# Kernel tuning notes

Hardware: AMD Instinct MI355X
Metric: run time of the kernel (lower is better)

The kernel has to match this reference:

```python
import jax, jax.numpy as jnp
import numpy as np
import math

B, T, C = 2, 2048, 1024
N_HEAD = 16
HEAD_DIM = C // N_HEAD


def setup_inputs() -> dict:
    key = jax.random.key(0)
    k1, k2, k3 = jax.random.split(key, 3)
    x = jax.random.normal(k1, (B, T, C), dtype=jnp.float32)
    # causal mask: positions where mask == 0 get -inf
    mask = jnp.tril(jnp.ones((T, T), dtype=bool))[None, None, :, :]
    W_attn = jax.random.normal(k2, (C, 3 * C), dtype=jnp.float32) * (1.0 / math.sqrt(C))
    b_attn = jnp.zeros((3 * C,), dtype=jnp.float32)
    W_proj = jax.random.normal(k3, (C, C), dtype=jnp.float32) * (1.0 / math.sqrt(C))
    b_proj = jnp.zeros((C,), dtype=jnp.float32)
    return {"x": x, "mask": mask, "W_attn": W_attn, "b_attn": b_attn,
            "W_proj": W_proj, "b_proj": b_proj}


def reference(x, mask, W_attn, b_attn, W_proj, b_proj):
    Bx, Tx, Cx = x.shape
    qkv = x @ W_attn + b_attn                      # [B,T,3C]
    q, k, v = jnp.split(qkv, 3, axis=2)
    # [B,T,C] -> [B,H,T,D]
    q = q.reshape(Bx, Tx, N_HEAD, HEAD_DIM).transpose(0, 2, 1, 3)
    k = k.reshape(Bx, Tx, N_HEAD, HEAD_DIM).transpose(0, 2, 1, 3)
    v = v.reshape(Bx, Tx, N_HEAD, HEAD_DIM).transpose(0, 2, 1, 3)
    scale = 1.0 / math.sqrt(HEAD_DIM)
    att = jnp.einsum('bhqd,bhkd->bhqk', q, k) * scale   # [B,H,T,T]
    att = jnp.where(mask, att, -jnp.inf)
    att = jax.nn.softmax(att, axis=-1)
    y = jnp.einsum('bhqk,bhkd->bhqd', att, v)            # [B,H,T,D]
    y = y.transpose(0, 2, 1, 3).reshape(Bx, Tx, Cx)      # [B,T,C]
    return y @ W_proj + b_proj
```

## Files before the change

### kernel.cpp

```cpp
#include <hip/hip_runtime.h>
#include <hip/hip_bf16.h>
#include <cstdint>

typedef unsigned short u16;
typedef unsigned int u32;
typedef unsigned long long u64;
using f32x4 = __attribute__((ext_vector_type(4))) float;
using s16x8 = __attribute__((ext_vector_type(8))) short;
using u32x4 = __attribute__((ext_vector_type(4))) u32;

#define NB 2
#define NT 2048
#define NC 1024
#define NH 16
#define HD 64

__device__ __forceinline__ u16 f2b(float f) {
    unsigned u = __float_as_uint(f);
    unsigned r = (u + 0x7FFFu + ((u >> 16) & 1u)) >> 16;
    return (u16)r;
}

__device__ __forceinline__ u32 cvtpk(float a, float b) {
    u32 r;
    asm("v_cvt_pk_bf16_f32 %0, %1, %2" : "=v"(r) : "v"(a), "v"(b));
    return r;
}
__device__ __forceinline__ void swap32(u32& a, u32& b) {
    asm("v_permlane32_swap_b32 %0, %1" : "+v"(a), "+v"(b));
}
__device__ __forceinline__ void swap16(u32& a, u32& b) {
    asm("v_permlane16_swap_b32 %0, %1" : "+v"(a), "+v"(b));
}

__device__ __forceinline__ void gl_lds16(const void* g, const void* l) {
    __builtin_amdgcn_global_load_lds(
        (const __attribute__((address_space(1))) unsigned int*)g,
        (__attribute__((address_space(3))) unsigned int*)l, 16, 0, 0);
}

__global__ __launch_bounds__(256) void conv_bf16(const float* __restrict__ in,
                                                 u16* __restrict__ out, int n4) {
    int i = blockIdx.x * 256 + threadIdx.x;
    if (i >= n4) return;
    float4 v = ((const float4*)in)[i];
    u64 pack = (u64)f2b(v.x) | ((u64)f2b(v.y) << 16) |
               ((u64)f2b(v.z) << 32) | ((u64)f2b(v.w) << 48);
    ((u64*)out)[i] = pack;
}

__global__ __launch_bounds__(256) void transpose_bf16(const float* __restrict__ W,
                                                      u16* __restrict__ Wt,
                                                      int K, int N) {
    __shared__ u16 s[64][65];
    const int n0 = blockIdx.x * 64, k0 = blockIdx.y * 64;
    const int t = threadIdx.x;
    const int tr = t >> 4, tc4 = (t & 15) * 4;
#pragma unroll
    for (int i = 0; i < 4; i++) {
        int r = tr + i * 16;
        float4 v = *(const float4*)&W[(size_t)(k0 + r) * N + n0 + tc4];
        s[r][tc4 + 0] = f2b(v.x);
        s[r][tc4 + 1] = f2b(v.y);
        s[r][tc4 + 2] = f2b(v.z);
        s[r][tc4 + 3] = f2b(v.w);
    }
    __syncthreads();
#pragma unroll
    for (int i = 0; i < 4; i++) {
        int nl = tr + i * 16;
        u64 pack = (u64)s[tc4 + 0][nl] | ((u64)s[tc4 + 1][nl] << 16) |
                   ((u64)s[tc4 + 2][nl] << 32) | ((u64)s[tc4 + 3][nl] << 48);
        *(u64*)&Wt[(size_t)(n0 + nl) * K + k0 + tc4] = pack;
    }
}

template <int OUT_BF16>
__global__ __launch_bounds__(256) void gemm_bt(const u16* __restrict__ A,
                                               const u16* __restrict__ Bt,
                                               const float* __restrict__ bias,
                                               void* __restrict__ Cout,
                                               int M, int N, int K) {
    __shared__ u16 As[128 * 32];
    __shared__ u16 Bs[128 * 32];
    const int tid = threadIdx.x;
    const int lane = tid & 63, w = tid >> 6;
    const int nx = gridDim.x;
    const int f = blockIdx.y * nx + blockIdx.x;
    const int qq = (nx * gridDim.y) >> 3;
    const int nid = (f & 7) * qq + (f >> 3);
    const int m0 = (nid / nx) * 128, n0 = (nid % nx) * 128;
    const int wm = w >> 1, wn = w & 1;
    f32x4 acc[4][4] = {};

    const int srow = 32 * w + (lane >> 2);
    const int scol = (lane & 3) * 8;

    for (int k0 = 0; k0 < K; k0 += 32) {
        gl_lds16(&A[(size_t)(m0 + srow) * K + k0 + scol], &As[w * 1024 + lane * 8]);
        gl_lds16(&A[(size_t)(m0 + srow + 16) * K + k0 + scol], &As[w * 1024 + 512 + lane * 8]);
        gl_lds16(&Bt[(size_t)(n0 + srow) * K + k0 + scol], &Bs[w * 1024 + lane * 8]);
        gl_lds16(&Bt[(size_t)(n0 + srow + 16) * K + k0 + scol], &Bs[w * 1024 + 512 + lane * 8]);
        __syncthreads();

        s16x8 af[4], bf[4];
#pragma unroll
        for (int mt = 0; mt < 4; mt++)
            af[mt] = *(const s16x8*)&As[(wm * 64 + mt * 16 + (lane & 15)) * 32 + (lane >> 4) * 8];
#pragma unroll
        for (int nt = 0; nt < 4; nt++)
            bf[nt] = *(const s16x8*)&Bs[(wn * 64 + nt * 16 + (lane & 15)) * 32 + (lane >> 4) * 8];
#pragma unroll
        for (int mt = 0; mt < 4; mt++)
#pragma unroll
            for (int nt = 0; nt < 4; nt++)
                acc[mt][nt] = __builtin_amdgcn_mfma_f32_16x16x32_bf16(af[mt], bf[nt], acc[mt][nt], 0, 0, 0);
        __syncthreads();
    }

#pragma unroll
    for (int mt = 0; mt < 4; mt++) {
        int row = m0 + wm * 64 + mt * 16 + (lane >> 4) * 4;
#pragma unroll
        for (int nt = 0; nt < 4; nt++) {
            int col = n0 + wn * 64 + nt * 16 + (lane & 15);
            float bs = bias[col];
#pragma unroll
            for (int r = 0; r < 4; r++) {
                float v = acc[mt][nt][r] + bs;
                if (OUT_BF16)
                    ((u16*)Cout)[(size_t)(row + r) * N + col] = f2b(v);
                else
                    ((float*)Cout)[(size_t)(row + r) * N + col] = v;
            }
        }
    }
}

__global__ __launch_bounds__(256) void gemm_bt_n64(const u16* __restrict__ A,
                                                   const u16* __restrict__ Bt,
                                                   const float* __restrict__ bias,
                                                   float* __restrict__ Cout,
                                                   int M, int N, int K) {
    __shared__ u16 As[128 * 32];
    __shared__ u16 Bs[64 * 32];
    const int tid = threadIdx.x;
    const int lane = tid & 63, w = tid >> 6;
    const int nx = gridDim.x;
    const int f = blockIdx.y * nx + blockIdx.x;
    const int qq = (nx * gridDim.y) >> 3;
    const int nid = (f & 7) * qq + (f >> 3);
    const int m0 = (nid / nx) * 128, n0 = (nid % nx) * 64;
    f32x4 acc[2][4] = {};

    const int srow = 32 * w + (lane >> 2);
    const int srowB = 16 * w + (lane >> 2);
    const int scol = (lane & 3) * 8;

    for (int k0 = 0; k0 < K; k0 += 32) {
        gl_lds16(&A[(size_t)(m0 + srow) * K + k0 + scol], &As[w * 1024 + lane * 8]);
        gl_lds16(&A[(size_t)(m0 + srow + 16) * K + k0 + scol], &As[w * 1024 + 512 + lane * 8]);
        gl_lds16(&Bt[(size_t)(n0 + srowB) * K + k0 + scol], &Bs[w * 512 + lane * 8]);
        __syncthreads();

        s16x8 af[2], bf[4];
#pragma unroll
        for (int mt = 0; mt < 2; mt++)
            af[mt] = *(const s16x8*)&As[(w * 32 + mt * 16 + (lane & 15)) * 32 + (lane >> 4) * 8];
#pragma unroll
        for (int nt = 0; nt < 4; nt++)
            bf[nt] = *(const s16x8*)&Bs[(nt * 16 + (lane & 15)) * 32 + (lane >> 4) * 8];
#pragma unroll
        for (int mt = 0; mt < 2; mt++)
#pragma unroll
            for (int nt = 0; nt < 4; nt++)
                acc[mt][nt] = __builtin_amdgcn_mfma_f32_16x16x32_bf16(af[mt], bf[nt], acc[mt][nt], 0, 0, 0);
        __syncthreads();
    }

#pragma unroll
    for (int mt = 0; mt < 2; mt++) {
        int row = m0 + w * 32 + mt * 16 + (lane >> 4) * 4;
#pragma unroll
        for (int nt = 0; nt < 4; nt++) {
            int col = n0 + nt * 16 + (lane & 15);
            float bs = bias[col];
#pragma unroll
            for (int r = 0; r < 4; r++)
                Cout[(size_t)(row + r) * N + col] = acc[mt][nt][r] + bs;
        }
    }
}

__global__ __launch_bounds__(256) void v_transpose(const u16* __restrict__ qkv,
                                                   u16* __restrict__ Vt) {
    __shared__ u16 s[64][65];
    const int t0 = blockIdx.x * 64;
    const int b = blockIdx.y >> 4, h = blockIdx.y & 15;
    const int t = threadIdx.x;
    const int tr = t >> 4, tc4 = (t & 15) * 4;
    const u16* src = qkv + (size_t)b * NT * (3 * NC) + 2 * NC + h * HD;
#pragma unroll
    for (int i = 0; i < 4; i++) {
        int r = tr + i * 16;
        u64 v = *(const u64*)&src[(size_t)(t0 + r) * (3 * NC) + tc4];
        s[r][tc4 + 0] = (u16)v;
        s[r][tc4 + 1] = (u16)(v >> 16);
        s[r][tc4 + 2] = (u16)(v >> 32);
        s[r][tc4 + 3] = (u16)(v >> 48);
    }
    __syncthreads();
    u16* dstb = Vt + (size_t)(b * NH + h) * HD * NT;
#pragma unroll
    for (int i = 0; i < 4; i++) {
        int d = tr + i * 16;
        u64 pack = (u64)s[tc4 + 0][d] | ((u64)s[tc4 + 1][d] << 16) |
                   ((u64)s[tc4 + 2][d] << 32) | ((u64)s[tc4 + 3][d] << 48);
        *(u64*)&dstb[(size_t)d * NT + t0 + tc4] = pack;
    }
}

__global__ __launch_bounds__(512) void attn_kernel(const u16* __restrict__ qkv,
                                                   const u16* __restrict__ Vt,
                                                   u16* __restrict__ yb) {
    __shared__ __align__(16) u16 Kb[2][2][64 * 64];
    __shared__ __align__(16) u16 Vb[2][2][64 * 64];

    const int l = threadIdx.x & 63;
    const int q16 = l & 15, g = l >> 4;
    const int wv = threadIdx.x >> 6;
    const int rg = wv & 3, hf = wv >> 2;
    const int i0 = blockIdx.x;
    const int xcd = i0 & 7, idx = i0 >> 3;
    const int hh = xcd * 4 + (idx >> 4);
    const int pr = idx & 15;
    const int b = hh >> 4, h = hh & 15;

    const u16* qkvb = qkv + (size_t)b * NT * (3 * NC);

    const int srow = l >> 3;
    const int sc8 = (l & 7) ^ (srow & 7);
    const u16* kSrc0 = qkvb + NC + h * HD + (size_t)(8 * rg + srow) * (3 * NC) + sc8 * 8;
    const u16* kSrc1 = kSrc0 + (size_t)32 * (3 * NC);
    const u16* vSrc0 = Vt + ((size_t)(b * NH + h) * HD + 8 * rg + srow) * NT + sc8 * 8;
    const u16* vSrc1 = vSrc0 + (size_t)32 * NT;
    const size_t kStep = (size_t)64 * (3 * NC);

    const float sc2 = 0.125f * 1.44269504088896340736f;
    const float SHIFT = 5.0f * 1.44269504088896340736f;
    const int sw = q16 & 7;

    u32 kfo[4][2], vfo[2][4];
#pragma unroll
    for (int ii = 0; ii < 4; ii++)
#pragma unroll
        for (int kc = 0; kc < 2; kc++)
            kfo[ii][kc] = (u32)(((16 * ii + q16) * 64 + ((4 * kc + g) ^ sw) * 8) * 2);
#pragma unroll
    for (int ks = 0; ks < 2; ks++)
#pragma unroll
        for (int dt = 0; dt < 4; dt++)
            vfo[ks][dt] = (u32)(((16 * dt + q16) * 64 + ((4 * ks + g) ^ sw) * 8) * 2);

#pragma unroll 1
    for (int sc = 0; sc < 2; ++sc) {
        const int cc = (sc == 0) ? (31 - pr) : pr;
        const int nt = cc + 1;
        const int h0 = (nt + 1) >> 1;
        const int base = hf ? h0 : 0;
        const int myN = hf ? (nt - h0) : h0;
        const int qw = cc * 64 + 16 * rg;

        s16x8 qf[2];
#pragma unroll
        for (int kc = 0; kc < 2; kc++)
            qf[kc] = *(const s16x8*)(qkvb + (size_t)(qw + q16) * (3 * NC) + h * HD + kc * 32 + g * 8);

        f32x4 yacc[4] = {};
        float lsum = 0.f;

        const u16* kP0 = kSrc0 + (size_t)base * kStep;
        const u16* kP1 = kSrc1 + (size_t)base * kStep;
        const u16* vP0 = vSrc0 + base * 64;
        const u16* vP1 = vSrc1 + base * 64;

        auto STAGE = [&](int buf) {
            gl_lds16(kP0, &Kb[hf][buf][rg * 512 + l * 8]);
            gl_lds16(kP1, &Kb[hf][buf][2048 + rg * 512 + l * 8]);
            gl_lds16(vP0, &Vb[hf][buf][rg * 512 + l * 8]);
            gl_lds16(vP1, &Vb[hf][buf][2048 + rg * 512 + l * 8]);
            kP0 += kStep; kP1 += kStep; vP0 += 64; vP1 += 64;
        };

        if (myN > 0) STAGE(base & 1);
        for (int u = 0; u < h0; ++u) {
            const int t = base + u;
            const bool act = (u < myN);
            __builtin_amdgcn_s_barrier();
            if (u + 1 < myN) {
                STAGE((t + 1) & 1);
                asm volatile("s_waitcnt vmcnt(4)" ::: "memory");
            } else {
                asm volatile("s_waitcnt vmcnt(0)" ::: "memory");
            }

            if (act) {
                const char* Kc = (const char*)&Kb[hf][t & 1][0];
                const char* Vc = (const char*)&Vb[hf][t & 1][0];

                s16x8 kf[4][2];
#pragma unroll
                for (int ii = 0; ii < 4; ii++)
#pragma unroll
                    for (int kc = 0; kc < 2; kc++)
                        kf[ii][kc] = *(const s16x8*)(Kc + kfo[ii][kc]);

                s16x8 vf0[4];
#pragma unroll
                for (int dt = 0; dt < 4; dt++)
                    vf0[dt] = *(const s16x8*)(Vc + vfo[0][dt]);

                f32x4 sacc[4] = {};
                __builtin_amdgcn_s_setprio(1);
#pragma unroll
                for (int ii = 0; ii < 4; ii++)
#pragma unroll
                    for (int kc = 0; kc < 2; kc++)
                        sacc[ii] = __builtin_amdgcn_mfma_f32_16x16x32_bf16(kf[ii][kc], qf[kc], sacc[ii], 0, 0, 0);
                __builtin_amdgcn_s_setprio(0);

                if (t == cc) {
                    const int kv0 = t * 64;
#pragma unroll
                    for (int ii = 0; ii < 4; ii++)
#pragma unroll
                        for (int r = 0; r < 4; r++)
                            if (kv0 + 16 * ii + 4 * g + r > qw + q16) sacc[ii][r] = -1e30f;
                }

                float p[4][4];
                float ps = 0.f;
#pragma unroll
                for (int ii = 0; ii < 4; ii++)
#pragma unroll
                    for (int r = 0; r < 4; r++) {
                        p[ii][r] = exp2f(fmaf(sacc[ii][r], sc2, -SHIFT));
                        ps += p[ii][r];
                    }
                lsum += ps;

                s16x8 pfrag[2];
#pragma unroll
                for (int ks = 0; ks < 2; ks++) {
                    u32 C0 = cvtpk(p[2 * ks][0], p[2 * ks][1]);
                    u32 C1 = cvtpk(p[2 * ks][2], p[2 * ks][3]);
                    u32 D0 = cvtpk(p[2 * ks + 1][0], p[2 * ks + 1][1]);
                    u32 D1 = cvtpk(p[2 * ks + 1][2], p[2 * ks + 1][3]);
                    swap32(C0, D0); swap16(C0, D0);
                    swap32(C1, D1); swap16(C1, D1);
                    u32x4 fr;
                    fr[0] = C0; fr[1] = C1; fr[2] = D0; fr[3] = D1;
                    pfrag[ks] = __builtin_bit_cast(s16x8, fr);
                }

                s16x8 vf1[4];
#pragma unroll
                for (int dt = 0; dt < 4; dt++)
                    vf1[dt] = *(const s16x8*)(Vc + vfo[1][dt]);

                __builtin_amdgcn_s_setprio(1);
#pragma unroll
                for (int dt = 0; dt < 4; dt++)
                    yacc[dt] = __builtin_amdgcn_mfma_f32_16x16x32_bf16(vf0[dt], pfrag[0], yacc[dt], 0, 0, 0);
#pragma unroll
                for (int dt = 0; dt < 4; dt++)
                    yacc[dt] = __builtin_amdgcn_mfma_f32_16x16x32_bf16(vf1[dt], pfrag[1], yacc[dt], 0, 0, 0);
                __builtin_amdgcn_s_setprio(0);
            }
        }
        __builtin_amdgcn_s_barrier();

        float* mY = (float*)&Kb[1][0][0];
        float* mL = (float*)&Vb[1][0][0];
        if (hf == 1) {
#pragma unroll
            for (int dt = 0; dt < 4; dt++)
#pragma unroll
                for (int r = 0; r < 4; r++)
                    mY[(rg * 16 + dt * 4 + r) * 64 + l] = yacc[dt][r];
            mL[rg * 64 + l] = lsum;
        }
        __syncthreads();
        if (hf == 0) {
#pragma unroll
            for (int dt = 0; dt < 4; dt++)
#pragma unroll
                for (int r = 0; r < 4; r++)
                    yacc[dt][r] += mY[(rg * 16 + dt * 4 + r) * 64 + l];
            lsum += mL[rg * 64 + l];
            lsum += __shfl_xor(lsum, 16);
            lsum += __shfl_xor(lsum, 32);
            float inv = 1.f / lsum;
            size_t rowoff = ((size_t)(b * NT + qw + q16)) * NC + h * HD;
#pragma unroll
            for (int dt = 0; dt < 4; dt++) {
                u32 lo = cvtpk(yacc[dt][0] * inv, yacc[dt][1] * inv);
                u32 hi = cvtpk(yacc[dt][2] * inv, yacc[dt][3] * inv);
                u64 pk = (u64)lo | ((u64)hi << 32);
                *(u64*)(yb + rowoff + 16 * dt + 4 * g) = pk;
            }
        }
        __syncthreads();
    }
}

extern "C" void kernel_launch(void* const* d_in, const int* in_sizes, int n_in,
                              void* d_out, int out_size, void* d_ws, size_t ws_size,
                              hipStream_t stream) {
    const float* x  = (const float*)d_in[0];
    const float* Wa = (const float*)d_in[2];
    const float* ba = (const float*)d_in[3];
    const float* Wp = (const float*)d_in[4];
    const float* bp = (const float*)d_in[5];
    float* out = (float*)d_out;

    char* ws = (char*)d_ws;
    u16* xb  = (u16*)(ws);
    u16* WaT = (u16*)(ws + (8ull << 20));
    u16* WpT = (u16*)(ws + (14ull << 20));
    u16* qkv = (u16*)(ws + (16ull << 20));
    u16* yb  = (u16*)(ws + (40ull << 20));
    u16* Vtb = (u16*)(ws + (48ull << 20));

    const int M = NB * NT;

    conv_bf16<<<(M * NC / 4 + 255) / 256, 256, 0, stream>>>(x, xb, M * NC / 4);
    transpose_bf16<<<dim3(3 * NC / 64, NC / 64), 256, 0, stream>>>(Wa, WaT, NC, 3 * NC);
    transpose_bf16<<<dim3(NC / 64, NC / 64), 256, 0, stream>>>(Wp, WpT, NC, NC);

    gemm_bt<1><<<dim3(3 * NC / 128, M / 128), 256, 0, stream>>>(xb, WaT, ba, qkv, M, 3 * NC, NC);

    v_transpose<<<dim3(NT / 64, NB * NH), 256, 0, stream>>>(qkv, Vtb);

    attn_kernel<<<dim3(NB * NH * 16), 512, 0, stream>>>(qkv, Vtb, yb);

    gemm_bt_n64<<<dim3(NC / 64, M / 128), 256, 0, stream>>>(yb, WpT, bp, out, M, NC, NC);
}
```

Baseline: 121.2 us.

## Double-buffer GEMM LDS tiles and reorder attention prefetch waits

Both GEMM kernels now use two LDS buffers and issue the global-to-LDS load for the next K-tile right after the barrier, so it overlaps the MFMA work on the current tile. Each iteration now needs one barrier instead of two, and the MFMA block is wrapped in s_setprio to raise wave priority during compute. The attention loop now waits for all outstanding loads before the barrier and issues the next stage afterward, instead of issuing and then waiting with vmcnt(4). The GEMMs double their LDS use, which may lower occupancy.

New measurement: 115.7 us. -4.5%, faster.

```diff
diff --git a/kernel.cpp b/kernel.cpp
--- a/kernel.cpp
+++ b/kernel.cpp
@@ -81,8 +81,8 @@
                                                const float* __restrict__ bias,
                                                void* __restrict__ Cout,
                                                int M, int N, int K) {
-    __shared__ u16 As[128 * 32];
-    __shared__ u16 Bs[128 * 32];
+    __shared__ u16 As[2][128 * 32];
+    __shared__ u16 Bs[2][128 * 32];
     const int tid = threadIdx.x;
     const int lane = tid & 63, w = tid >> 6;
     const int nx = gridDim.x;
@@ -95,39 +95,55 @@
 
     const int srow = 32 * w + (lane >> 2);
     const int scol = (lane & 3) * 8;
-
-    for (int k0 = 0; k0 < K; k0 += 32) {
-        gl_lds16(&A[(size_t)(m0 + srow) * K + k0 + scol], &As[w * 1024 + lane * 8]);
-        gl_lds16(&A[(size_t)(m0 + srow + 16) * K + k0 + scol], &As[w * 1024 + 512 + lane * 8]);
-        gl_lds16(&Bt[(size_t)(n0 + srow) * K + k0 + scol], &Bs[w * 1024 + lane * 8]);
-        gl_lds16(&Bt[(size_t)(n0 + srow + 16) * K + k0 + scol], &Bs[w * 1024 + 512 + lane * 8]);
-        __syncthreads();
-
+    const u16* aP0 = &A[(size_t)(m0 + srow) * K + scol];
+    const u16* aP1 = aP0 + (size_t)16 * K;
+    const u16* bP0 = &Bt[(size_t)(n0 + srow) * K + scol];
+    const u16* bP1 = bP0 + (size_t)16 * K;
+
+    auto STAGE = [&](int t) {
+        const int buf = t & 1;
+        const int k0 = t * 32;
+        gl_lds16(aP0 + k0, &As[buf][w * 1024 + lane * 8]);
+        gl_lds16(aP1 + k0, &As[buf][w * 1024 + 512 + lane * 8]);
+        gl_lds16(bP0 + k0, &Bs[buf][w * 1024 + lane * 8]);
+        gl_lds16(bP1 + k0, &Bs[buf][w * 1024 + 512 + lane * 8]);
+    };
+
+    const int nt = K >> 5;
+    STAGE(0);
+    for (int t = 0; t < nt; ++t) {
+        asm volatile("s_waitcnt vmcnt(0)" ::: "memory");
+        __builtin_amdgcn_s_barrier();
+        if (t + 1 < nt) STAGE(t + 1);
+
+        const u16* Asb = As[t & 1];
+        const u16* Bsb = Bs[t & 1];
         s16x8 af[4], bf[4];
 #pragma unroll
         for (int mt = 0; mt < 4; mt++)
-            af[mt] = *(const s16x8*)&As[(wm * 64 + mt * 16 + (lane & 15)) * 32 + (lane >> 4) * 8];
-#pragma unroll
-        for (int nt = 0; nt < 4; nt++)
-            bf[nt] = *(const s16x8*)&Bs[(wn * 64 + nt * 16 + (lane & 15)) * 32 + (lane >> 4) * 8];
+            af[mt] = *(const s16x8*)&Asb[(wm * 64 + mt * 16 + (lane & 15)) * 32 + (lane >> 4) * 8];
+#pragma unroll
+        for (int nt2 = 0; nt2 < 4; nt2++)
+            bf[nt2] = *(const s16x8*)&Bsb[(wn * 64 + nt2 * 16 + (lane & 15)) * 32 + (lane >> 4) * 8];
+        __builtin_amdgcn_s_setprio(1);
 #pragma unroll
         for (int mt = 0; mt < 4; mt++)
 #pragma unroll
-            for (int nt = 0; nt < 4; nt++)
-                acc[mt][nt] = __builtin_amdgcn_mfma_f32_16x16x32_bf16(af[mt], bf[nt], acc[mt][nt], 0, 0, 0);
-        __syncthreads();
+            for (int nt2 = 0; nt2 < 4; nt2++)
+                acc[mt][nt2] = __builtin_amdgcn_mfma_f32_16x16x32_bf16(af[mt], bf[nt2], acc[mt][nt2], 0, 0, 0);
+        __builtin_amdgcn_s_setprio(0);
     }
 
 #pragma unroll
     for (int mt = 0; mt < 4; mt++) {
         int row = m0 + wm * 64 + mt * 16 + (lane >> 4) * 4;
 #pragma unroll
-        for (int nt = 0; nt < 4; nt++) {
-            int col = n0 + wn * 64 + nt * 16 + (lane & 15);
+        for (int nt2 = 0; nt2 < 4; nt2++) {
+            int col = n0 + wn * 64 + nt2 * 16 + (lane & 15);
             float bs = bias[col];
 #pragma unroll
             for (int r = 0; r < 4; r++) {
-                float v = acc[mt][nt][r] + bs;
+                float v = acc[mt][nt2][r] + bs;
                 if (OUT_BF16)
                     ((u16*)Cout)[(size_t)(row + r) * N + col] = f2b(v);
                 else
@@ -142,8 +158,8 @@
                                                    const float* __restrict__ bias,
                                                    float* __restrict__ Cout,
                                                    int M, int N, int K) {
-    __shared__ u16 As[128 * 32];
-    __shared__ u16 Bs[64 * 32];
+    __shared__ u16 As[2][128 * 32];
+    __shared__ u16 Bs[2][64 * 32];
     const int tid = threadIdx.x;
     const int lane = tid & 63, w = tid >> 6;
     const int nx = gridDim.x;
@@ -156,38 +172,53 @@
     const int srow = 32 * w + (lane >> 2);
     const int srowB = 16 * w + (lane >> 2);
     const int scol = (lane & 3) * 8;
-
-    for (int k0 = 0; k0 < K; k0 += 32) {
-        gl_lds16(&A[(size_t)(m0 + srow) * K + k0 + scol], &As[w * 1024 + lane * 8]);
-        gl_lds16(&A[(size_t)(m0 + srow + 16) * K + k0 + scol], &As[w * 1024 + 512 + lane * 8]);
-        gl_lds16(&Bt[(size_t)(n0 + srowB) * K + k0 + scol], &Bs[w * 512 + lane * 8]);
-        __syncthreads();
-
+    const u16* aP0 = &A[(size_t)(m0 + srow) * K + scol];
+    const u16* aP1 = aP0 + (size_t)16 * K;
+    const u16* bP0 = &Bt[(size_t)(n0 + srowB) * K + scol];
+
+    auto STAGE = [&](int t) {
+        const int buf = t & 1;
+        const int k0 = t * 32;
+        gl_lds16(aP0 + k0, &As[buf][w * 1024 + lane * 8]);
+        gl_lds16(aP1 + k0, &As[buf][w * 1024 + 512 + lane * 8]);
+        gl_lds16(bP0 + k0, &Bs[buf][w * 512 + lane * 8]);
+    };
+
+    const int nt = K >> 5;
+    STAGE(0);
+    for (int t = 0; t < nt; ++t) {
+        asm volatile("s_waitcnt vmcnt(0)" ::: "memory");
+        __builtin_amdgcn_s_barrier();
+        if (t + 1 < nt) STAGE(t + 1);
+
+        const u16* Asb = As[t & 1];
+        const u16* Bsb = Bs[t & 1];
         s16x8 af[2], bf[4];
 #pragma unroll
         for (int mt = 0; mt < 2; mt++)
-            af[mt] = *(const s16x8*)&As[(w * 32 + mt * 16 + (lane & 15)) * 32 + (lane >> 4) * 8];
-#pragma unroll
-        for (int nt = 0; nt < 4; nt++)
-            bf[nt] = *(const s16x8*)&Bs[(nt * 16 + (lane & 15)) * 32 + (lane >> 4) * 8];
+            af[mt] = *(const s16x8*)&Asb[(w * 32 + mt * 16 + (lane & 15)) * 32 + (lane >> 4) * 8];
+#pragma unroll
+        for (int nt2 = 0; nt2 < 4; nt2++)
+            bf[nt2] = *(const s16x8*)&Bsb[(nt2 * 16 + (lane & 15)) * 32 + (lane >> 4) * 8];
+        __builtin_amdgcn_s_setprio(1);
 #pragma unroll
         for (int mt = 0; mt < 2; mt++)
 #pragma unroll
-            for (int nt = 0; nt < 4; nt++)
-                acc[mt][nt] = __builtin_amdgcn_mfma_f32_16x16x32_bf16(af[mt], bf[nt], acc[mt][nt], 0, 0, 0);
-        __syncthreads();
+            for (int nt2 = 0; nt2 < 4; nt2++)
+                acc[mt][nt2] = __builtin_amdgcn_mfma_f32_16x16x32_bf16(af[mt], bf[nt2], acc[mt][nt2], 0, 0, 0);
+        __builtin_amdgcn_s_setprio(0);
     }
 
 #pragma unroll
     for (int mt = 0; mt < 2; mt++) {
         int row = m0 + w * 32 + mt * 16 + (lane >> 4) * 4;
 #pragma unroll
-        for (int nt = 0; nt < 4; nt++) {
-            int col = n0 + nt * 16 + (lane & 15);
+        for (int nt2 = 0; nt2 < 4; nt2++) {
+            int col = n0 + nt2 * 16 + (lane & 15);
             float bs = bias[col];
 #pragma unroll
             for (int r = 0; r < 4; r++)
-                Cout[(size_t)(row + r) * N + col] = acc[mt][nt][r] + bs;
+                Cout[(size_t)(row + r) * N + col] = acc[mt][nt2][r] + bs;
         }
     }
 }
@@ -296,13 +327,9 @@
         for (int u = 0; u < h0; ++u) {
             const int t = base + u;
             const bool act = (u < myN);
+            asm volatile("s_waitcnt vmcnt(0)" ::: "memory");
             __builtin_amdgcn_s_barrier();
-            if (u + 1 < myN) {
-                STAGE((t + 1) & 1);
-                asm volatile("s_waitcnt vmcnt(4)" ::: "memory");
-            } else {
-                asm volatile("s_waitcnt vmcnt(0)" ::: "memory");
-            }
+            if (u + 1 < myN) STAGE((t + 1) & 1);
 
             if (act) {
                 const char* Kc = (const char*)&Kb[hf][t & 1][0];
```
